# Optimization experiments

Measured on AMD Instinct MI355X. Metric: run time of the kernel, lower is better.

The kernel has to match this reference:

```python
import jax, jax.numpy as jnp
import numpy as np

GAMMA = 0.99
GAE_LAMBDA = 0.95
DONE_PROB = 0.01  # sparse episode terminations, typical for long-horizon trading envs


def setup_inputs() -> dict:
    key = jax.random.key(0)
    k1, k2, k3 = jax.random.split(key, 3)
    T, N = 2048, 4096  # rollout_len, num_envs
    rewards = jax.random.normal(k1, (T, N), dtype=jnp.float32)
    values = jax.random.normal(k2, (T, N), dtype=jnp.float32)
    dones = (jax.random.uniform(k3, (T, N)) < DONE_PROB).astype(jnp.float32)
    return {"rewards": rewards, "values": values, "dones": dones}


def reference(rewards, values, dones):
    # rewards/values/dones: [T, N]
    T, N = rewards.shape
    # bootstrap: beyond the last step, next_value = 0 and next_done = 1
    next_value = jnp.concatenate([values[1:], jnp.zeros((1, N), values.dtype)], axis=0)
    next_done = jnp.concatenate([dones[1:], jnp.ones((1, N), dones.dtype)], axis=0)
    nonterminal = 1.0 - next_done                      # [T, N]
    delta = rewards + GAMMA * next_value * nonterminal - values  # [T, N]

    def step(last_adv, xs):
        d, nt = xs                                     # each [N]
        adv = d + GAMMA * GAE_LAMBDA * nt * last_adv
        return adv, adv

    init = jnp.zeros((N,), rewards.dtype)
    _, advantages = jax.lax.scan(step, init, (delta, nonterminal), reverse=True)
    returns = advantages + values
    return advantages, returns
```

## Files before the change

### kernel.cpp

```cpp
#include <hip/hip_runtime.h>


#define T_LEN    2048
#define N_ENV    4096
#define NV2      (N_ENV / 2)
#define N_CHUNKS 128
#define CHUNK_L  (T_LEN / N_CHUNKS)

typedef float v2f __attribute__((ext_vector_type(2)));

static constexpr float GAMMA = 0.99f;
static constexpr float GL    = 0.99f * 0.95f;

__global__ __launch_bounds__(256) void gae_phase1(
    const v2f* __restrict__ rewards,
    const v2f* __restrict__ values,
    const v2f* __restrict__ dones,
    v2f* __restrict__ Aout,
    v2f* __restrict__ Pout)
{
    const int idx = blockIdx.x * blockDim.x + threadIdx.x;
    const int n2 = idx & (NV2 - 1);
    const int c  = idx >> 11;
    const int t_hi = c * CHUNK_L + (CHUNK_L - 1);

    v2f v_next, d_next;
    if (c == N_CHUNKS - 1) {
        v_next = (v2f)(0.f, 0.f);
        d_next = (v2f)(1.f, 1.f);
    } else {
        v_next = values[(t_hi + 1) * NV2 + n2];
        d_next = dones [(t_hi + 1) * NV2 + n2];
    }

    v2f A = (v2f)(1.f, 1.f);
    v2f P = (v2f)(0.f, 0.f);

    #pragma unroll
    for (int i = 0; i < CHUNK_L; ++i) {
        const int t = t_hi - i;
        const v2f r = rewards[t * NV2 + n2];
        const v2f v = values [t * NV2 + n2];
        const v2f d = dones  [t * NV2 + n2];
        #define STEP(X) { \
            const float nt    = 1.0f - d_next.X; \
            const float delta = fmaf(GAMMA * v_next.X, nt, r.X) - v.X; \
            const float cc    = GL * nt; \
            P.X = fmaf(cc, P.X, delta); \
            A.X = cc * A.X; \
            v_next.X = v.X; d_next.X = d.X; }
        STEP(x) STEP(y)
        #undef STEP
    }
    Aout[idx] = A;
    Pout[idx] = P;
}

__global__ __launch_bounds__(256) void gae_phase23(
    const v2f* __restrict__ rewards,
    const v2f* __restrict__ values,
    const v2f* __restrict__ dones,
    const v2f* __restrict__ Ain,
    const v2f* __restrict__ Pin,
    v2f* __restrict__ out)
{
    const int idx = blockIdx.x * blockDim.x + threadIdx.x;
    const int n2 = idx & (NV2 - 1);
    const int c  = idx >> 11;
    const int t_hi = c * CHUNK_L + (CHUNK_L - 1);

    v2f adv = (v2f)(0.f, 0.f);
    #pragma unroll 8
    for (int c2 = N_CHUNKS - 1; c2 > c; --c2) {
        const v2f a = Ain[c2 * NV2 + n2];
        const v2f p = Pin[c2 * NV2 + n2];
        adv.x = fmaf(a.x, adv.x, p.x);
        adv.y = fmaf(a.y, adv.y, p.y);
    }

    v2f v_next, d_next;
    if (c == N_CHUNKS - 1) {
        v_next = (v2f)(0.f, 0.f);
        d_next = (v2f)(1.f, 1.f);
    } else {
        v_next = values[(t_hi + 1) * NV2 + n2];
        d_next = dones [(t_hi + 1) * NV2 + n2];
    }

    #pragma unroll
    for (int i = 0; i < CHUNK_L; ++i) {
        const int t = t_hi - i;
        const v2f r = rewards[t * NV2 + n2];
        const v2f v = values [t * NV2 + n2];
        const v2f d = dones  [t * NV2 + n2];
        v2f ret;
        #define STEP(X) { \
            const float nt    = 1.0f - d_next.X; \
            const float delta = fmaf(GAMMA * v_next.X, nt, r.X) - v.X; \
            const float cc    = GL * nt; \
            adv.X = fmaf(cc, adv.X, delta); \
            ret.X = adv.X + v.X; \
            v_next.X = v.X; d_next.X = d.X; }
        STEP(x) STEP(y)
        #undef STEP
        __builtin_nontemporal_store(adv, &out[t * NV2 + n2]);
        __builtin_nontemporal_store(ret, &out[(T_LEN + t) * NV2 + n2]);
    }
}

extern "C" void kernel_launch(void* const* d_in, const int* in_sizes, int n_in,
                              void* d_out, int out_size, void* d_ws, size_t ws_size,
                              hipStream_t stream) {
    const v2f* rewards = (const v2f*)d_in[0];
    const v2f* values  = (const v2f*)d_in[1];
    const v2f* dones   = (const v2f*)d_in[2];
    v2f* out = (v2f*)d_out;

    v2f* A = (v2f*)d_ws;
    v2f* P = A + (size_t)N_CHUNKS * NV2;

    const int blk = 256;
    gae_phase1<<<(N_CHUNKS * NV2) / blk, blk, 0, stream>>>(
        rewards, values, dones, A, P);
    gae_phase23<<<(N_CHUNKS * NV2) / blk, blk, 0, stream>>>(
        rewards, values, dones, A, P, out);
}
```

Baseline: 172.8 us.

## Add hierarchical group-level carry composition to shorten the serial prefix loop

Adds an intermediate kernel that composes the per-chunk affine carries (A,P) into groups of 8 chunks. Phase 2/3 then combines at most 15 group carries plus up to 7 chunk carries, instead of up to 127 chunk carries per thread. This cuts the redundant serial prefix reads and FMAs that grow with chunk index. In exchange it adds a third kernel launch and extra workspace traffic.

```diff
diff --git a/kernel.cpp b/kernel.cpp
--- a/kernel.cpp
+++ b/kernel.cpp
@@ -6,6 +6,8 @@
 #define NV2      (N_ENV / 2)
 #define N_CHUNKS 128
 #define CHUNK_L  (T_LEN / N_CHUNKS)
+#define GRP_SZ   8
+#define N_GRPS   (N_CHUNKS / GRP_SZ)
 
 typedef float v2f __attribute__((ext_vector_type(2)));
 
@@ -56,22 +58,58 @@
     Pout[idx] = P;
 }
 
+__global__ __launch_bounds__(256) void gae_phase1b(
+    const v2f* __restrict__ Ain,
+    const v2f* __restrict__ Pin,
+    v2f* __restrict__ GAout,
+    v2f* __restrict__ GPout)
+{
+    const int idx = blockIdx.x * blockDim.x + threadIdx.x;
+    const int n2 = idx & (NV2 - 1);
+    const int g  = idx >> 11;
+    const int hi = g * GRP_SZ + (GRP_SZ - 1);
+
+    v2f GA = (v2f)(1.f, 1.f);
+    v2f GP = (v2f)(0.f, 0.f);
+    #pragma unroll
+    for (int i = 0; i < GRP_SZ; ++i) {
+        const int c2 = hi - i;
+        const v2f a = Ain[c2 * NV2 + n2];
+        const v2f p = Pin[c2 * NV2 + n2];
+        GP.x = fmaf(a.x, GP.x, p.x);
+        GP.y = fmaf(a.y, GP.y, p.y);
+        GA.x = a.x * GA.x;
+        GA.y = a.y * GA.y;
+    }
+    GAout[idx] = GA;
+    GPout[idx] = GP;
+}
+
 __global__ __launch_bounds__(256) void gae_phase23(
     const v2f* __restrict__ rewards,
     const v2f* __restrict__ values,
     const v2f* __restrict__ dones,
     const v2f* __restrict__ Ain,
     const v2f* __restrict__ Pin,
+    const v2f* __restrict__ GAin,
+    const v2f* __restrict__ GPin,
     v2f* __restrict__ out)
 {
     const int idx = blockIdx.x * blockDim.x + threadIdx.x;
     const int n2 = idx & (NV2 - 1);
     const int c  = idx >> 11;
+    const int g  = c / GRP_SZ;
+    const int gend = g * GRP_SZ + (GRP_SZ - 1);
     const int t_hi = c * CHUNK_L + (CHUNK_L - 1);
 
     v2f adv = (v2f)(0.f, 0.f);
-    #pragma unroll 8
-    for (int c2 = N_CHUNKS - 1; c2 > c; --c2) {
+    for (int g2 = N_GRPS - 1; g2 > g; --g2) {
+        const v2f a = GAin[g2 * NV2 + n2];
+        const v2f p = GPin[g2 * NV2 + n2];
+        adv.x = fmaf(a.x, adv.x, p.x);
+        adv.y = fmaf(a.y, adv.y, p.y);
+    }
+    for (int c2 = gend; c2 > c; --c2) {
         const v2f a = Ain[c2 * NV2 + n2];
         const v2f p = Pin[c2 * NV2 + n2];
         adv.x = fmaf(a.x, adv.x, p.x);
@@ -116,12 +154,15 @@
     const v2f* dones   = (const v2f*)d_in[2];
     v2f* out = (v2f*)d_out;
 
-    v2f* A = (v2f*)d_ws;
-    v2f* P = A + (size_t)N_CHUNKS * NV2;
+    v2f* A  = (v2f*)d_ws;
+    v2f* P  = A  + (size_t)N_CHUNKS * NV2;
+    v2f* GA = P  + (size_t)N_CHUNKS * NV2;
+    v2f* GP = GA + (size_t)N_GRPS  * NV2;
 
     const int blk = 256;
     gae_phase1<<<(N_CHUNKS * NV2) / blk, blk, 0, stream>>>(
         rewards, values, dones, A, P);
+    gae_phase1b<<<(N_GRPS * NV2) / blk, blk, 0, stream>>>(A, P, GA, GP);
     gae_phase23<<<(N_CHUNKS * NV2) / blk, blk, 0, stream>>>(
-        rewards, values, dones, A, P, out);
+        rewards, values, dones, A, P, GA, GP, out);
 }
```

After: 165.3 us. 1.05x faster.
